# Kernel optimization log

Measured on AMD Instinct MI355X. Metric: run time of the kernel, lower is better.

The kernel has to match this reference:

```python
import jax, jax.numpy as jnp
import numpy as np

K_TOP = 2
N_HEADS = 4

def _ln(x, g, b, eps=1e-5):
    mu = x.mean(-1, keepdims=True)
    var = ((x - mu) ** 2).mean(-1, keepdims=True)
    return (x - mu) * jax.lax.rsqrt(var + eps) * g + b

def setup_inputs() -> dict:
    key = jax.random.key(0)
    ks = jax.random.split(key, 12)
    B, Na, dz, da = 1024, 32, 96, 32
    D = dz + da
    E, F, Hh, nr = 8, 1024, 512, 4
    s = 0.02
    rn = lambda k, sh: jax.random.normal(k, sh, jnp.float32) * s
    return dict(
        z=jax.random.normal(ks[0], (B, Na, dz), jnp.float32),
        a=jax.random.normal(ks[1], (B, Na, da), jnp.float32),
        w_gate=rn(ks[2], (Na * D, E)),
        w_in=rn(ks[3], (E, 3 * D, D)), b_in=jnp.zeros((E, 3 * D), jnp.float32),
        w_out=rn(ks[4], (E, D, D)), b_out=jnp.zeros((E, D), jnp.float32),
        ln1_g=jnp.ones((E, D), jnp.float32), ln1_b=jnp.zeros((E, D), jnp.float32),
        w1=rn(ks[5], (E, F, D)), b1=jnp.zeros((E, F), jnp.float32),
        w2=rn(ks[6], (E, D, F)), b2=jnp.zeros((E, D), jnp.float32),
        ln2_g=jnp.ones((E, D), jnp.float32), ln2_b=jnp.zeros((E, D), jnp.float32),
        head_w1=rn(ks[7], (Hh, Na * D)), head_b1=jnp.zeros((Hh,), jnp.float32),
        head_w2=rn(ks[8], (nr, Hh)), head_b2=jnp.zeros((nr,), jnp.float32),
    )

def reference(z, a, w_gate, w_in, b_in, w_out, b_out, ln1_g, ln1_b, w1, b1, w2, b2, ln2_g, ln2_b, head_w1, head_b1, head_w2, head_b2):
    B, Na, _ = z.shape
    x = jnp.concatenate([z, a], axis=-1)          # [B, Na, D]
    D = x.shape[-1]
    E = w_gate.shape[1]
    hd = D // N_HEADS
    x_flat = x.reshape(B, -1)                     # [B, Na*D]

    # --- NoisyTopKRouter (eval: clean logits only) ---
    logits = x_flat @ w_gate                      # [B, E]
    top_vals, top_idx = jax.lax.top_k(logits, min(K_TOP + 1, E))
    tk_gates = jax.nn.softmax(top_vals[:, :K_TOP], axis=1)
    gates = jnp.zeros_like(logits).at[jnp.arange(B)[:, None], top_idx[:, :K_TOP]].set(tk_gates)
    load = (gates > 0).sum(0).astype(jnp.float32)
    importance = gates.sum(0)
    cv2 = lambda v: jnp.var(v, ddof=1) / (jnp.mean(v) ** 2 + 1e-10)
    loss_bal = cv2(importance) + cv2(load) + jax.scipy.special.logsumexp(logits, axis=-1).mean()

    # --- expert (self-attn + FFN, pre/post-LN residual) ---
    def expert(p):
        wi, bi, wo, bo, g1, be1, W1, B1, W2, B2, g2, be2 = p
        qkv = x @ wi.T + bi                       # [B, Na, 3D]
        q, k_, v = jnp.split(qkv, 3, axis=-1)
        q = q.reshape(B, Na, N_HEADS, hd)
        k_ = k_.reshape(B, Na, N_HEADS, hd)
        v = v.reshape(B, Na, N_HEADS, hd)
        sc = jnp.einsum('bqhd,bkhd->bhqk', q, k_) / jnp.sqrt(jnp.float32(hd))
        att = jax.nn.softmax(sc, axis=-1)
        o = jnp.einsum('bhqk,bkhd->bqhd', att, v).reshape(B, Na, D)
        o = o @ wo.T + bo
        h = _ln(x + o, g1, be1)
        f = jax.nn.relu(h @ W1.T + B1) @ W2.T + B2
        return _ln(h + f, g2, be2)

    def body(y, p):
        *ep, gate_e = p                           # gate_e: [B]
        y = y + gate_e[:, None, None] * expert(tuple(ep))
        return y, None

    xs = (w_in, b_in, w_out, b_out, ln1_g, ln1_b, w1, b1, w2, b2, ln2_g, ln2_b, gates.T)
    y, _ = jax.lax.scan(body, jnp.zeros_like(x), xs)

    y_flat = y.reshape(B, -1)
    r = jax.nn.relu(y_flat @ head_w1.T + head_b1) @ head_w2.T + head_b2  # [B, n_r]
    return r, gates, loss_bal
```

## Files before the change

### kernel.cpp

```cpp
#include <hip/hip_runtime.h>
#include <math.h>


typedef short bf16x8 __attribute__((ext_vector_type(8)));
typedef float f32x4 __attribute__((ext_vector_type(4)));
typedef unsigned short u16;

#define MFMA(a, b, c) __builtin_amdgcn_mfma_f32_16x16x32_bf16((a), (b), (c), 0, 0, 0)

__device__ __forceinline__ u16 f2bf(float f) {
    unsigned int u = __float_as_uint(f);
    unsigned int r = u + 0x7FFFu + ((u >> 16) & 1u);
    return (u16)(r >> 16);
}
__device__ __forceinline__ float bf2f(u16 s) {
    return __uint_as_float(((unsigned int)s) << 16);
}

__global__ __launch_bounds__(256) void convert_kernel(
    const float* __restrict__ wi, const float* __restrict__ wo,
    const float* __restrict__ w1, const float* __restrict__ w2,
    const float* __restrict__ hw1,
    u16* __restrict__ wiB, u16* __restrict__ woB, u16* __restrict__ w1B,
    u16* __restrict__ w2B, u16* __restrict__ hw1B)
{
    int i4 = blockIdx.x * 256 + threadIdx.x;
    int e = i4 * 4;
    const float* s; u16* d; int off;
    if (e < 393216)       { s = wi;  d = wiB;  off = e; }
    else if (e < 524288)  { s = wo;  d = woB;  off = e - 393216; }
    else if (e < 1572864) { s = w1;  d = w1B;  off = e - 524288; }
    else if (e < 2621440) { s = w2;  d = w2B;  off = e - 1572864; }
    else                  { s = hw1; d = hw1B; off = e - 2621440; }
    float4 v = *(const float4*)(s + off);
    ushort4 o;
    o.x = f2bf(v.x); o.y = f2bf(v.y); o.z = f2bf(v.z); o.w = f2bf(v.w);
    *(ushort4*)(d + off) = o;
}

__global__ __launch_bounds__(256) void router_kernel(
    const float* __restrict__ z, const float* __restrict__ a,
    const float* __restrict__ wg,
    float* __restrict__ gates_out, float* __restrict__ lse_ws,
    int* __restrict__ topi, float* __restrict__ topg)
{
    __shared__ float red[256][9];
    const int b = blockIdx.x, t = threadIdx.x;
    float acc[8];
#pragma unroll
    for (int e = 0; e < 8; ++e) acc[e] = 0.f;
#pragma unroll
    for (int i = 0; i < 16; ++i) {
        int f = i * 256 + t;
        int n = f >> 7, d = f & 127;
        float xv = (d < 96) ? z[(b * 32 + n) * 96 + d]
                            : a[(b * 32 + n) * 32 + d - 96];
        const float* wr = wg + f * 8;
#pragma unroll
        for (int e = 0; e < 8; ++e) acc[e] += xv * wr[e];
    }
#pragma unroll
    for (int e = 0; e < 8; ++e) red[t][e] = acc[e];
    __syncthreads();
    for (int s = 128; s; s >>= 1) {
        if (t < s) {
#pragma unroll
            for (int e = 0; e < 8; ++e) red[t][e] += red[t + s][e];
        }
        __syncthreads();
    }
    if (t == 0) {
        float L[8];
#pragma unroll
        for (int e = 0; e < 8; ++e) L[e] = red[0][e];
        int i0 = 0;
#pragma unroll
        for (int e = 1; e < 8; ++e) if (L[e] > L[i0]) i0 = e;
        int i1 = -1; float v1 = -3.0e38f;
#pragma unroll
        for (int e = 0; e < 8; ++e) if (e != i0 && L[e] > v1) { v1 = L[e]; i1 = e; }
        float e1 = expf(v1 - L[i0]);
        float inv = 1.f / (1.f + e1);
        float g0 = inv, g1 = e1 * inv;
#pragma unroll
        for (int e = 0; e < 8; ++e)
            gates_out[b * 8 + e] = (e == i0) ? g0 : ((e == i1) ? g1 : 0.f);
        float m = L[i0];
        float se = 0.f;
#pragma unroll
        for (int e = 0; e < 8; ++e) se += expf(L[e] - m);
        lse_ws[b] = m + logf(se);
        topi[b * 2 + 0] = i0; topi[b * 2 + 1] = i1;
        topg[b * 2 + 0] = g0; topg[b * 2 + 1] = g1;
    }
}

__global__ __launch_bounds__(1024) void build_loss_kernel(
    const int* __restrict__ topi, const float* __restrict__ topg,
    const float* __restrict__ lse,
    int* __restrict__ cnts, int* __restrict__ ent, float* __restrict__ out_loss)
{
    __shared__ int sc_[8];
    __shared__ float red[9][1024];
    const int t = threadIdx.x;
    if (t < 8) sc_[t] = 0;
    __syncthreads();
    int e0 = topi[t * 2], e1 = topi[t * 2 + 1];
    float g0 = topg[t * 2], g1 = topg[t * 2 + 1];
    int p0 = atomicAdd(&sc_[e0], 1);
    ent[e0 * 2048 + p0] = t * 2;
    int p1 = atomicAdd(&sc_[e1], 1);
    ent[e1 * 2048 + p1] = t * 2 + 1;
#pragma unroll
    for (int e = 0; e < 8; ++e)
        red[e][t] = ((e == e0) ? g0 : 0.f) + ((e == e1) ? g1 : 0.f);
    red[8][t] = lse[t];
    __syncthreads();
    for (int s = 512; s; s >>= 1) {
        if (t < s) {
#pragma unroll
            for (int q = 0; q < 9; ++q) red[q][t] += red[q][t + s];
        }
        __syncthreads();
    }
    if (t == 0) {
        float cvv[2];
        for (int p = 0; p < 2; ++p) {
            float v[8], sum = 0.f;
            for (int e = 0; e < 8; ++e) {
                v[e] = p ? (float)sc_[e] : red[e][0];
                sum += v[e];
            }
            float mean = sum * (1.f / 8.f);
            float var = 0.f;
            for (int e = 0; e < 8; ++e) { float d = v[e] - mean; var += d * d; }
            var *= (1.f / 7.f);
            cvv[p] = var / (mean * mean + 1e-10f);
        }
        out_loss[0] = cvv[0] + cvv[1] + red[8][0] * (1.f / 1024.f);
    }
    __syncthreads();
    if (t < 8) cnts[t] = sc_[t];
}

#define SM_X 0
#define SM_Q 16384
#define SM_K 32768
#define SM_V 49152
#define SM_TOT 65536
#define PS_OFF 0
#define PQ_OFF 1024
#define MU_OFF 2048
#define RS_OFF 2304
#define ATTN_GRID 8192

__device__ __forceinline__ int tsw(int row, int col) {
    return row * 256 + ((col * 2) ^ ((row & 7) << 4));
}
__device__ __forceinline__ int vsw(int row, int col) {
    return row * 128 + ((col * 2) ^ ((row & 7) << 4));
}

__global__ __launch_bounds__(512, 2) void attn_kernel(
    const float* __restrict__ z, const float* __restrict__ a,
    const u16* __restrict__ wiBF, const float* __restrict__ b_in,
    const u16* __restrict__ woBF, const float* __restrict__ b_out,
    const float* __restrict__ ln1g, const float* __restrict__ ln1b,
    const int* __restrict__ cnts, const int* __restrict__ ent,
    u16* __restrict__ h1g)
{
    const int e = blockIdx.x & 7, j = blockIdx.x >> 3;
    const int cnt = cnts[e];
    if (j * 2 >= cnt) return;
    const int base = j * 2;

    __shared__ __align__(16) char sm[SM_TOT];
    const int t = threadIdx.x;
    const int w = t >> 6, l = t & 63, l16 = l & 15, lk = l >> 4;
    const int ke = lk * 8;
    const int wr = w >> 2, wc = w & 3;
    const f32x4 zv = {0.f, 0.f, 0.f, 0.f};

    int bs[2];
#pragma unroll
    for (int i = 0; i < 2; ++i) {
        int gi = base + i;
        int idx = (gi < cnt) ? gi : (cnt - 1);
        bs[i] = ent[e * 2048 + idx];
    }

#pragma unroll
    for (int i = 0; i < 2; ++i) {
        int cid = i * 512 + t;
        int row = cid >> 4;
        int cb = (cid & 15) * 8;
        int b_ = bs[row >> 5] >> 1;
        int n = row & 31;
        float4 p0, p1;
        if (cb < 96) {
            const float* zp = z + ((size_t)b_ * 32 + n) * 96 + cb;
            p0 = *(const float4*)zp; p1 = *(const float4*)(zp + 4);
        } else {
            const float* ap = a + ((size_t)b_ * 32 + n) * 32 + (cb - 96);
            p0 = *(const float4*)ap; p1 = *(const float4*)(ap + 4);
        }
        bf16x8 pk;
        pk[0] = (short)f2bf(p0.x); pk[1] = (short)f2bf(p0.y);
        pk[2] = (short)f2bf(p0.z); pk[3] = (short)f2bf(p0.w);
        pk[4] = (short)f2bf(p1.x); pk[5] = (short)f2bf(p1.y);
        pk[6] = (short)f2bf(p1.z); pk[7] = (short)f2bf(p1.w);
        *(bf16x8*)(sm + SM_X + tsw(row, cb)) = pk;
    }
    __syncthreads();

    {
        f32x4 acc[2][6];
#pragma unroll
        for (int mt = 0; mt < 2; ++mt)
#pragma unroll
            for (int q = 0; q < 6; ++q) acc[mt][q] = zv;
#pragma unroll
        for (int ks = 0; ks < 4; ++ks) {
            bf16x8 af[2];
#pragma unroll
            for (int mt = 0; mt < 2; ++mt) {
                int R = wr * 32 + mt * 16 + l16;
                af[mt] = *(const bf16x8*)(sm + SM_X + tsw(R, ks * 32 + ke));
            }
#pragma unroll
            for (int q = 0; q < 6; ++q) {
                int jj = wc * 96 + q * 16 + l16;
                bf16x8 bb = *(const bf16x8*)(wiBF + e * 49152 + jj * 128 + ks * 32 + ke);
#pragma unroll
                for (int mt = 0; mt < 2; ++mt) acc[mt][q] = MFMA(af[mt], bb, acc[mt][q]);
            }
        }
#pragma unroll
        for (int q = 0; q < 6; ++q) {
            int C = wc * 96 + q * 16 + l16;
            float bj = b_in[e * 384 + C];
#pragma unroll
            for (int mt = 0; mt < 2; ++mt)
#pragma unroll
                for (int i = 0; i < 4; ++i) {
                    int R = wr * 32 + mt * 16 + lk * 4 + i;
                    u16 val = f2bf(acc[mt][q][i] + bj);
                    if (C < 128) {
                        *(u16*)(sm + SM_Q + tsw(R, C)) = val;
                    } else if (C < 256) {
                        *(u16*)(sm + SM_K + tsw(R, C - 128)) = val;
                    } else {
                        *(u16*)(sm + SM_V + vsw(C - 256, R)) = val;
                    }
                }
        }
    }
    __syncthreads();

    {
        const int tok = w >> 2, hb = (w & 3) * 32;
        const float scale = 0.17677669529663687f;
        bf16x8 qa[2], kf[2];
#pragma unroll
        for (int mt = 0; mt < 2; ++mt) {
            int R = tok * 32 + mt * 16 + l16;
            qa[mt] = *(const bf16x8*)(sm + SM_Q + tsw(R, hb + ke));
            kf[mt] = *(const bf16x8*)(sm + SM_K + tsw(R, hb + ke));
        }
        f32x4 sc[2][2];
        sc[0][0] = MFMA(qa[0], kf[0], zv); sc[0][1] = MFMA(qa[0], kf[1], zv);
        sc[1][0] = MFMA(qa[1], kf[0], zv); sc[1][1] = MFMA(qa[1], kf[1], zv);
#pragma unroll
        for (int mt = 0; mt < 2; ++mt)
#pragma unroll
            for (int i = 0; i < 4; ++i) {
                float v0 = sc[mt][0][i] * scale, v1 = sc[mt][1][i] * scale;
                float m = fmaxf(v0, v1);
                m = fmaxf(m, __shfl_xor(m, 1)); m = fmaxf(m, __shfl_xor(m, 2));
                m = fmaxf(m, __shfl_xor(m, 4)); m = fmaxf(m, __shfl_xor(m, 8));
                float e0 = __expf(v0 - m), e1 = __expf(v1 - m);
                float ssum = e0 + e1;
                ssum += __shfl_xor(ssum, 1); ssum += __shfl_xor(ssum, 2);
                ssum += __shfl_xor(ssum, 4); ssum += __shfl_xor(ssum, 8);
                float inv = 1.f / ssum;
                int row = mt * 16 + lk * 4 + i;
                char* pb = sm + SM_X + w * 2048 + row * 64;
                int sw = (row & 3) << 4;
                *(u16*)(pb + ((l16 * 2) ^ sw)) = f2bf(e0 * inv);
                *(u16*)(pb + (((16 + l16) * 2) ^ sw)) = f2bf(e1 * inv);
            }
        bf16x8 pa[2];
#pragma unroll
        for (int mt = 0; mt < 2; ++mt) {
            int row = mt * 16 + l16;
            pa[mt] = *(const bf16x8*)(sm + SM_X + w * 2048 + row * 64 +
                                      ((ke * 2) ^ ((row & 3) << 4)));
        }
        f32x4 o[2][2];
#pragma unroll
        for (int nt = 0; nt < 2; ++nt) {
            int rv = hb + nt * 16 + l16;
            bf16x8 vb = *(const bf16x8*)(sm + SM_V + vsw(rv, tok * 32 + ke));
            o[0][nt] = MFMA(pa[0], vb, zv);
            o[1][nt] = MFMA(pa[1], vb, zv);
        }
#pragma unroll
        for (int mt = 0; mt < 2; ++mt)
#pragma unroll
            for (int nt = 0; nt < 2; ++nt)
#pragma unroll
                for (int i = 0; i < 4; ++i) {
                    int R = tok * 32 + mt * 16 + lk * 4 + i;
                    int C = hb + nt * 16 + l16;
                    *(u16*)(sm + SM_Q + tsw(R, C)) = f2bf(o[mt][nt][i]);
                }
    }
    __syncthreads();

    {
        f32x4 pr[2][2];
        pr[0][0] = zv; pr[0][1] = zv; pr[1][0] = zv; pr[1][1] = zv;
#pragma unroll
        for (int ks = 0; ks < 4; ++ks) {
            bf16x8 af[2];
#pragma unroll
            for (int mt = 0; mt < 2; ++mt) {
                int R = wr * 32 + mt * 16 + l16;
                af[mt] = *(const bf16x8*)(sm + SM_Q + tsw(R, ks * 32 + ke));
            }
#pragma unroll
            for (int nt = 0; nt < 2; ++nt) {
                int jj = wc * 32 + nt * 16 + l16;
                bf16x8 bb = *(const bf16x8*)(woBF + e * 16384 + jj * 128 + ks * 32 + ke);
                pr[0][nt] = MFMA(af[0], bb, pr[0][nt]);
                pr[1][nt] = MFMA(af[1], bb, pr[1][nt]);
            }
        }
        int C0 = wc * 32 + l16, C1 = C0 + 16;
        float bo0 = b_out[e * 128 + C0];
        float bo1 = b_out[e * 128 + C1];
        int b_ = bs[wr] >> 1;
#pragma unroll
        for (int mt = 0; mt < 2; ++mt)
#pragma unroll
            for (int i = 0; i < 4; ++i) {
                int R = wr * 32 + mt * 16 + lk * 4 + i;
                int n = R & 31;
                float x0 = (C0 < 96) ? z[((size_t)b_ * 32 + n) * 96 + C0]
                                     : a[((size_t)b_ * 32 + n) * 32 + C0 - 96];
                float x1 = (C1 < 96) ? z[((size_t)b_ * 32 + n) * 96 + C1]
                                     : a[((size_t)b_ * 32 + n) * 32 + C1 - 96];
                float u0 = pr[mt][0][i] + bo0 + x0;
                float u1v = pr[mt][1][i] + bo1 + x1;
                *(u16*)(sm + SM_K + tsw(R, C0)) = f2bf(u0);
                *(u16*)(sm + SM_K + tsw(R, C1)) = f2bf(u1v);
                float s = u0 + u1v;
                float q = u0 * u0 + u1v * u1v;
                s += __shfl_xor(s, 1); q += __shfl_xor(q, 1);
                s += __shfl_xor(s, 2); q += __shfl_xor(q, 2);
                s += __shfl_xor(s, 4); q += __shfl_xor(q, 4);
                s += __shfl_xor(s, 8); q += __shfl_xor(q, 8);
                if (l16 == 0) {
                    *(float*)(sm + SM_X + PS_OFF + (R * 4 + wc) * 4) = s;
                    *(float*)(sm + SM_X + PQ_OFF + (R * 4 + wc) * 4) = q;
                }
            }
    }
    __syncthreads();
    if (t < 64) {
        float s = 0.f, q = 0.f;
#pragma unroll
        for (int c = 0; c < 4; ++c) {
            s += *(const float*)(sm + SM_X + PS_OFF + (t * 4 + c) * 4);
            q += *(const float*)(sm + SM_X + PQ_OFF + (t * 4 + c) * 4);
        }
        float mu = s * (1.f / 128.f);
        float var = q * (1.f / 128.f) - mu * mu;
        *(float*)(sm + SM_X + MU_OFF + t * 4) = mu;
        *(float*)(sm + SM_X + RS_OFF + t * 4) = rsqrtf(var + 1e-5f);
    }
    __syncthreads();
    {
        int r_ = t >> 3, c0 = (t & 7) * 16;
        float mu_ = *(const float*)(sm + SM_X + MU_OFF + r_ * 4);
        float rs_ = *(const float*)(sm + SM_X + RS_OFF + r_ * 4);
#pragma unroll
        for (int j4 = 0; j4 < 2; ++j4) {
            int cb = c0 + j4 * 8;
            bf16x8* p = (bf16x8*)(sm + SM_K + tsw(r_, cb));
            bf16x8 vch = *p;
#pragma unroll
            for (int jj = 0; jj < 8; ++jj) {
                int c = cb + jj;
                float f = (bf2f((u16)vch[jj]) - mu_) * rs_ * ln1g[e * 128 + c] + ln1b[e * 128 + c];
                vch[jj] = (short)f2bf(f);
            }
            *p = vch;
        }
    }
    __syncthreads();
#pragma unroll
    for (int i = 0; i < 2; ++i) {
        int cid = i * 512 + t;
        int r_ = cid >> 4, cb = (cid & 15) * 8;
        int code = bs[r_ >> 5];
        u16* dst = h1g + (size_t)code * 4096 + (r_ & 31) * 128 + cb;
        *(bf16x8*)dst = *(const bf16x8*)(sm + SM_K + tsw(r_, cb));
    }
}

#define FH 0
#define FF 32768
#define FPS 65536
#define FPQ 67584
#define FMU 69632
#define FRS 70144
#define F_TOT 70656
#define FFN_GRID 4096

__global__ __launch_bounds__(512, 2) void ffn_kernel(
    const u16* __restrict__ h1g,
    const u16* __restrict__ w1BF, const float* __restrict__ b1,
    const u16* __restrict__ w2BF, const float* __restrict__ b2,
    const float* __restrict__ ln2g, const float* __restrict__ ln2b,
    const float* __restrict__ topg, const int* __restrict__ cnts,
    const int* __restrict__ ent,
    u16* __restrict__ ybf)
{
    const int e = blockIdx.x & 7, jt = blockIdx.x >> 3;
    const int cnt = cnts[e];
    if (jt * 4 >= cnt) return;
    const int base = jt * 4;

    __shared__ __align__(16) char sm[F_TOT];
    const int t = threadIdx.x;
    const int w = t >> 6, l = t & 63, l16 = l & 15, lk = l >> 4;
    const int ke = lk * 8;
    const int wr = w >> 2, wc = w & 3;
    const f32x4 zv = {0.f, 0.f, 0.f, 0.f};

    int code4[4]; float gg4[4];
#pragma unroll
    for (int i = 0; i < 4; ++i) {
        int gi = base + i;
        int idx = (gi < cnt) ? gi : (cnt - 1);
        code4[i] = ent[e * 2048 + idx];
        gg4[i] = topg[code4[i]];
    }

#pragma unroll
    for (int it = 0; it < 4; ++it) {
        int cid = it * 512 + t;
        int row = cid >> 4, cb = (cid & 15) * 8;
        int code = code4[row >> 5];
        *(bf16x8*)(sm + FH + tsw(row, cb)) =
            *(const bf16x8*)(h1g + (size_t)code * 4096 + (row & 31) * 128 + cb);
    }
    __syncthreads();

    f32x4 facc[4][2];
#pragma unroll
    for (int mt = 0; mt < 4; ++mt) { facc[mt][0] = zv; facc[mt][1] = zv; }

    for (int c = 0; c < 8; ++c) {
        f32x4 a1[4][2];
#pragma unroll
        for (int mt = 0; mt < 4; ++mt) { a1[mt][0] = zv; a1[mt][1] = zv; }
#pragma unroll
        for (int ks = 0; ks < 4; ++ks) {
            bf16x8 af[4];
#pragma unroll
            for (int mt = 0; mt < 4; ++mt) {
                int R = wr * 64 + mt * 16 + l16;
                af[mt] = *(const bf16x8*)(sm + FH + tsw(R, ks * 32 + ke));
            }
#pragma unroll
            for (int nt = 0; nt < 2; ++nt) {
                int jj = c * 128 + wc * 32 + nt * 16 + l16;
                bf16x8 bb = *(const bf16x8*)(w1BF + e * 131072 + jj * 128 + ks * 32 + ke);
#pragma unroll
                for (int mt = 0; mt < 4; ++mt) a1[mt][nt] = MFMA(af[mt], bb, a1[mt][nt]);
            }
        }
        __syncthreads();
#pragma unroll
        for (int nt = 0; nt < 2; ++nt) {
            int C = wc * 32 + nt * 16 + l16;
            float bv = b1[e * 1024 + c * 128 + C];
#pragma unroll
            for (int mt = 0; mt < 4; ++mt)
#pragma unroll
                for (int i = 0; i < 4; ++i) {
                    int R = wr * 64 + mt * 16 + lk * 4 + i;
                    *(u16*)(sm + FF + tsw(R, C)) = f2bf(fmaxf(a1[mt][nt][i] + bv, 0.f));
                }
        }
        __syncthreads();
#pragma unroll
        for (int ks = 0; ks < 4; ++ks) {
            bf16x8 af[4];
#pragma unroll
            for (int mt = 0; mt < 4; ++mt) {
                int R = wr * 64 + mt * 16 + l16;
                af[mt] = *(const bf16x8*)(sm + FF + tsw(R, ks * 32 + ke));
            }
#pragma unroll
            for (int nt = 0; nt < 2; ++nt) {
                int jj = wc * 32 + nt * 16 + l16;
                bf16x8 bb = *(const bf16x8*)(w2BF + e * 131072 + jj * 1024 +
                                             c * 128 + ks * 32 + ke);
#pragma unroll
                for (int mt = 0; mt < 4; ++mt) facc[mt][nt] = MFMA(af[mt], bb, facc[mt][nt]);
            }
        }
    }
    __syncthreads();

    {
        int C0 = wc * 32 + l16, C1 = C0 + 16;
        float b20 = b2[e * 128 + C0];
        float b21 = b2[e * 128 + C1];
#pragma unroll
        for (int mt = 0; mt < 4; ++mt)
#pragma unroll
            for (int i = 0; i < 4; ++i) {
                int R = wr * 64 + mt * 16 + lk * 4 + i;
                float h0 = bf2f(*(const u16*)(sm + FH + tsw(R, C0)));
                float h1v = bf2f(*(const u16*)(sm + FH + tsw(R, C1)));
                float u0 = facc[mt][0][i] + b20 + h0;
                float u1v = facc[mt][1][i] + b21 + h1v;
                *(u16*)(sm + FF + tsw(R, C0)) = f2bf(u0);
                *(u16*)(sm + FF + tsw(R, C1)) = f2bf(u1v);
                float s = u0 + u1v;
                float q = u0 * u0 + u1v * u1v;
                s += __shfl_xor(s, 1); q += __shfl_xor(q, 1);
                s += __shfl_xor(s, 2); q += __shfl_xor(q, 2);
                s += __shfl_xor(s, 4); q += __shfl_xor(q, 4);
                s += __shfl_xor(s, 8); q += __shfl_xor(q, 8);
                if (l16 == 0) {
                    *(float*)(sm + FPS + (R * 4 + wc) * 4) = s;
                    *(float*)(sm + FPQ + (R * 4 + wc) * 4) = q;
                }
            }
    }
    __syncthreads();
    if (t < 128) {
        float s = 0.f, q = 0.f;
#pragma unroll
        for (int c = 0; c < 4; ++c) {
            s += *(const float*)(sm + FPS + (t * 4 + c) * 4);
            q += *(const float*)(sm + FPQ + (t * 4 + c) * 4);
        }
        float mu = s * (1.f / 128.f);
        float var = q * (1.f / 128.f) - mu * mu;
        *(float*)(sm + FMU + t * 4) = mu;
        *(float*)(sm + FRS + t * 4) = rsqrtf(var + 1e-5f);
    }
    __syncthreads();
#pragma unroll
    for (int it = 0; it < 4; ++it) {
        int cid = it * 512 + t;
        int row = cid >> 4, cb = (cid & 15) * 8;
        float mu = *(const float*)(sm + FMU + row * 4);
        float rs = *(const float*)(sm + FRS + row * 4);
        int ei = row >> 5;
        float gm = gg4[ei];
        int code = code4[ei];
        int tok = code >> 1, slot = code & 1;
        bf16x8 v = *(const bf16x8*)(sm + FF + tsw(row, cb));
        bf16x8 o;
#pragma unroll
        for (int jj = 0; jj < 8; ++jj) {
            int cc = cb + jj;
            float f = (bf2f((u16)v[jj]) - mu) * rs * ln2g[e * 128 + cc] + ln2b[e * 128 + cc];
            o[jj] = (short)f2bf(gm * f);
        }
        *(bf16x8*)(ybf + (size_t)(slot * 1024 + tok) * 4096 + (row & 31) * 128 + cb) = o;
    }
}

__global__ __launch_bounds__(256) void combine_kernel(
    u16* __restrict__ y0, const u16* __restrict__ y1)
{
    int i = (blockIdx.x * 256 + threadIdx.x) * 8;
    bf16x8 a = *(const bf16x8*)(y0 + i);
    bf16x8 b = *(const bf16x8*)(y1 + i);
    bf16x8 o;
#pragma unroll
    for (int j = 0; j < 8; ++j)
        o[j] = (short)f2bf(bf2f((u16)a[j]) + bf2f((u16)b[j]));
    *(bf16x8*)(y0 + i) = o;
}

__global__ __launch_bounds__(256) void head1_mfma(
    const u16* __restrict__ y_bf, const u16* __restrict__ hw1BF,
    const float* __restrict__ hb1, float* __restrict__ h_act)
{
    const int t = threadIdx.x, w = t >> 6, l = t & 63, l16 = l & 15, lk = l >> 4;
    const int ke = lk * 8;
    const int mb = blockIdx.x * 32, cb = blockIdx.y * 64 + w * 16;
    const f32x4 zv = {0.f, 0.f, 0.f, 0.f};
    f32x4 acc[2]; acc[0] = zv; acc[1] = zv;
    const u16* arow0 = y_bf + (size_t)(mb + l16) * 4096;
    const u16* arow1 = y_bf + (size_t)(mb + 16 + l16) * 4096;
    const u16* brow  = hw1BF + (size_t)(cb + l16) * 4096;
    for (int k0 = 0; k0 < 4096; k0 += 32) {
        bf16x8 a0 = *(const bf16x8*)(arow0 + k0 + ke);
        bf16x8 a1 = *(const bf16x8*)(arow1 + k0 + ke);
        bf16x8 bb = *(const bf16x8*)(brow + k0 + ke);
        acc[0] = MFMA(a0, bb, acc[0]);
        acc[1] = MFMA(a1, bb, acc[1]);
    }
    int col = cb + l16;
    float bv = hb1[col];
#pragma unroll
    for (int mt = 0; mt < 2; ++mt)
#pragma unroll
        for (int i = 0; i < 4; ++i) {
            int row = mb + mt * 16 + lk * 4 + i;
            h_act[(size_t)row * 512 + col] = fmaxf(acc[mt][i] + bv, 0.f);
        }
}

__global__ __launch_bounds__(64) void head2_kernel(
    const float* __restrict__ h_act, const float* __restrict__ w2,
    const float* __restrict__ b2, float* __restrict__ r)
{
    const int b = blockIdx.x, t = threadIdx.x;
    float a0 = 0.f, a1 = 0.f, a2 = 0.f, a3 = 0.f;
    for (int h = t; h < 512; h += 64) {
        float hv = h_act[b * 512 + h];
        a0 += hv * w2[h];
        a1 += hv * w2[512 + h];
        a2 += hv * w2[1024 + h];
        a3 += hv * w2[1536 + h];
    }
#pragma unroll
    for (int off = 32; off; off >>= 1) {
        a0 += __shfl_down(a0, off);
        a1 += __shfl_down(a1, off);
        a2 += __shfl_down(a2, off);
        a3 += __shfl_down(a3, off);
    }
    if (t == 0) {
        r[b * 4 + 0] = a0 + b2[0];
        r[b * 4 + 1] = a1 + b2[1];
        r[b * 4 + 2] = a2 + b2[2];
        r[b * 4 + 3] = a3 + b2[3];
    }
}

extern "C" void kernel_launch(void* const* d_in, const int* in_sizes, int n_in,
                              void* d_out, int out_size, void* d_ws, size_t ws_size,
                              hipStream_t stream) {
    const float* z    = (const float*)d_in[0];
    const float* a    = (const float*)d_in[1];
    const float* wg   = (const float*)d_in[2];
    const float* w_in = (const float*)d_in[3];
    const float* b_in = (const float*)d_in[4];
    const float* w_o  = (const float*)d_in[5];
    const float* b_o  = (const float*)d_in[6];
    const float* l1g  = (const float*)d_in[7];
    const float* l1b  = (const float*)d_in[8];
    const float* w1   = (const float*)d_in[9];
    const float* b1   = (const float*)d_in[10];
    const float* w2   = (const float*)d_in[11];
    const float* b2   = (const float*)d_in[12];
    const float* l2g  = (const float*)d_in[13];
    const float* l2b  = (const float*)d_in[14];
    const float* hw1  = (const float*)d_in[15];
    const float* hb1  = (const float*)d_in[16];
    const float* hw2  = (const float*)d_in[17];
    const float* hb2  = (const float*)d_in[18];

    float* out = (float*)d_out;
    float* r_out     = out;
    float* gates_out = out + 4096;
    float* loss_out  = out + 12288;

    char* W = (char*)d_ws;
    u16*   wiBF  = (u16*)(W + 0);
    u16*   woBF  = (u16*)(W + 786432);
    u16*   w1BF  = (u16*)(W + 1048576);
    u16*   w2BF  = (u16*)(W + 3145728);
    u16*   hw1BF = (u16*)(W + 5242880);
    u16*   ybf   = (u16*)(W + 9437184);
    u16*   h1g   = (u16*)(W + 26214400);
    float* h_act = (float*)(W + 42991616);
    float* lse   = (float*)(W + 45088768);
    float* topg  = (float*)(W + 45092864);
    int*   topi  = (int*)  (W + 45101056);
    int*   cnts  = (int*)  (W + 45109248);
    int*   ent   = (int*)  (W + 45109376);

    convert_kernel<<<4608, 256, 0, stream>>>(w_in, w_o, w1, w2, hw1,
                                             wiBF, woBF, w1BF, w2BF, hw1BF);
    router_kernel<<<1024, 256, 0, stream>>>(z, a, wg, gates_out, lse, topi, topg);
    build_loss_kernel<<<1, 1024, 0, stream>>>(topi, topg, lse, cnts, ent, loss_out);
    attn_kernel<<<ATTN_GRID, 512, 0, stream>>>(z, a, wiBF, b_in, woBF, b_o,
        l1g, l1b, cnts, ent, h1g);
    ffn_kernel<<<FFN_GRID, 512, 0, stream>>>(h1g, w1BF, b1, w2BF, b2,
        l2g, l2b, topg, cnts, ent, ybf);
    combine_kernel<<<2048, 256, 0, stream>>>(ybf, ybf + 4194304);
    head1_mfma<<<dim3(32, 8), 256, 0, stream>>>(ybf, hw1BF, hb1, h_act);
    head2_kernel<<<1024, 64, 0, stream>>>(h_act, hw2, hb2, r_out);
}
```

Before: 320.9 us.

## Restructure FFN kernel to keep full 1024-wide hidden activations in LDS

The FFN kernel now handles 2 entries (64 rows) per block instead of 4 (128 rows). It computes the whole 64x1024 ReLU hidden layer into shared memory in one pass, with each wave owning 128 hidden columns, and then runs the second GEMM over K=1024 without the per-chunk barriers. This removes the two __syncthreads per hidden chunk and the interleaving of the two GEMMs. The cost is about 146KB of LDS per block, so occupancy drops to one block per CU despite launch_bounds(512,2). Each block also reuses its streamed weights across half as many rows, which doubles total weight traffic.

After: 322.9 us. Within noise of the previous version (+0.6%).

```diff
diff --git a/kernel.cpp b/kernel.cpp
--- a/kernel.cpp
+++ b/kernel.cpp
@@ -159,6 +159,9 @@
 }
 __device__ __forceinline__ int vsw(int row, int col) {
     return row * 128 + ((col * 2) ^ ((row & 7) << 4));
+}
+__device__ __forceinline__ int fsw(int row, int col) {
+    return row * 2048 + ((col * 2) ^ ((row & 7) << 4));
 }
 
 __global__ __launch_bounds__(512, 2) void attn_kernel(
@@ -410,13 +413,13 @@
 }
 
 #define FH 0
-#define FF 32768
-#define FPS 65536
-#define FPQ 67584
-#define FMU 69632
-#define FRS 70144
-#define F_TOT 70656
-#define FFN_GRID 4096
+#define FFB 16384
+#define FPS 147456
+#define FPQ 148480
+#define FMU 149504
+#define FRS 149760
+#define F_TOT 150016
+#define FFN_GRID 8192
 
 __global__ __launch_bounds__(512, 2) void ffn_kernel(
     const u16* __restrict__ h1g,
@@ -429,8 +432,8 @@
 {
     const int e = blockIdx.x & 7, jt = blockIdx.x >> 3;
     const int cnt = cnts[e];
-    if (jt * 4 >= cnt) return;
-    const int base = jt * 4;
+    if (jt * 2 >= cnt) return;
+    const int base = jt * 2;
 
     __shared__ __align__(16) char sm[F_TOT];
     const int t = threadIdx.x;
@@ -439,79 +442,75 @@
     const int wr = w >> 2, wc = w & 3;
     const f32x4 zv = {0.f, 0.f, 0.f, 0.f};
 
-    int code4[4]; float gg4[4];
-#pragma unroll
-    for (int i = 0; i < 4; ++i) {
+    int code2[2]; float gg2[2];
+#pragma unroll
+    for (int i = 0; i < 2; ++i) {
         int gi = base + i;
         int idx = (gi < cnt) ? gi : (cnt - 1);
-        code4[i] = ent[e * 2048 + idx];
-        gg4[i] = topg[code4[i]];
-    }
-
-#pragma unroll
-    for (int it = 0; it < 4; ++it) {
+        code2[i] = ent[e * 2048 + idx];
+        gg2[i] = topg[code2[i]];
+    }
+
+#pragma unroll
+    for (int it = 0; it < 2; ++it) {
         int cid = it * 512 + t;
         int row = cid >> 4, cb = (cid & 15) * 8;
-        int code = code4[row >> 5];
+        int code = code2[row >> 5];
         *(bf16x8*)(sm + FH + tsw(row, cb)) =
             *(const bf16x8*)(h1g + (size_t)code * 4096 + (row & 31) * 128 + cb);
     }
     __syncthreads();
 
-    f32x4 facc[4][2];
-#pragma unroll
-    for (int mt = 0; mt < 4; ++mt) { facc[mt][0] = zv; facc[mt][1] = zv; }
-
-    for (int c = 0; c < 8; ++c) {
-        f32x4 a1[4][2];
-#pragma unroll
-        for (int mt = 0; mt < 4; ++mt) { a1[mt][0] = zv; a1[mt][1] = zv; }
+    for (int h = 0; h < 4; ++h) {
+        f32x4 acc[4][2];
+#pragma unroll
+        for (int mf = 0; mf < 4; ++mf) { acc[mf][0] = zv; acc[mf][1] = zv; }
 #pragma unroll
         for (int ks = 0; ks < 4; ++ks) {
             bf16x8 af[4];
 #pragma unroll
-            for (int mt = 0; mt < 4; ++mt) {
-                int R = wr * 64 + mt * 16 + l16;
-                af[mt] = *(const bf16x8*)(sm + FH + tsw(R, ks * 32 + ke));
-            }
-#pragma unroll
-            for (int nt = 0; nt < 2; ++nt) {
-                int jj = c * 128 + wc * 32 + nt * 16 + l16;
+            for (int mf = 0; mf < 4; ++mf) {
+                int R = mf * 16 + l16;
+                af[mf] = *(const bf16x8*)(sm + FH + tsw(R, ks * 32 + ke));
+            }
+#pragma unroll
+            for (int nf = 0; nf < 2; ++nf) {
+                int jj = w * 128 + h * 32 + nf * 16 + l16;
                 bf16x8 bb = *(const bf16x8*)(w1BF + e * 131072 + jj * 128 + ks * 32 + ke);
 #pragma unroll
-                for (int mt = 0; mt < 4; ++mt) a1[mt][nt] = MFMA(af[mt], bb, a1[mt][nt]);
-            }
-        }
-        __syncthreads();
-#pragma unroll
-        for (int nt = 0; nt < 2; ++nt) {
-            int C = wc * 32 + nt * 16 + l16;
-            float bv = b1[e * 1024 + c * 128 + C];
-#pragma unroll
-            for (int mt = 0; mt < 4; ++mt)
+                for (int mf = 0; mf < 4; ++mf) acc[mf][nf] = MFMA(af[mf], bb, acc[mf][nf]);
+            }
+        }
+#pragma unroll
+        for (int nf = 0; nf < 2; ++nf) {
+            int C = w * 128 + h * 32 + nf * 16 + l16;
+            float bv = b1[e * 1024 + C];
+#pragma unroll
+            for (int mf = 0; mf < 4; ++mf)
 #pragma unroll
                 for (int i = 0; i < 4; ++i) {
-                    int R = wr * 64 + mt * 16 + lk * 4 + i;
-                    *(u16*)(sm + FF + tsw(R, C)) = f2bf(fmaxf(a1[mt][nt][i] + bv, 0.f));
+                    int R = mf * 16 + lk * 4 + i;
+                    *(u16*)(sm + FFB + fsw(R, C)) = f2bf(fmaxf(acc[mf][nf][i] + bv, 0.f));
                 }
         }
-        __syncthreads();
-#pragma unroll
-        for (int ks = 0; ks < 4; ++ks) {
-            bf16x8 af[4];
-#pragma unroll
-            for (int mt = 0; mt < 4; ++mt) {
-                int R = wr * 64 + mt * 16 + l16;
-                af[mt] = *(const bf16x8*)(sm + FF + tsw(R, ks * 32 + ke));
-            }
-#pragma unroll
-            for (int nt = 0; nt < 2; ++nt) {
-                int jj = wc * 32 + nt * 16 + l16;
-                bf16x8 bb = *(const bf16x8*)(w2BF + e * 131072 + jj * 1024 +
-                                             c * 128 + ks * 32 + ke);
-#pragma unroll
-                for (int mt = 0; mt < 4; ++mt) facc[mt][nt] = MFMA(af[mt], bb, facc[mt][nt]);
-            }
+    }
+    __syncthreads();
+
+    f32x4 cacc[2][2];
+    cacc[0][0] = zv; cacc[0][1] = zv; cacc[1][0] = zv; cacc[1][1] = zv;
+    for (int ks = 0; ks < 32; ++ks) {
+        bf16x8 af[2];
+#pragma unroll
+        for (int mt = 0; mt < 2; ++mt) {
+            int R = wr * 32 + mt * 16 + l16;
+            af[mt] = *(const bf16x8*)(sm + FFB + fsw(R, ks * 32 + ke));
+        }
+#pragma unroll
+        for (int nf = 0; nf < 2; ++nf) {
+            int jj = wc * 32 + nf * 16 + l16;
+            bf16x8 bb = *(const bf16x8*)(w2BF + e * 131072 + jj * 1024 + ks * 32 + ke);
+            cacc[0][nf] = MFMA(af[0], bb, cacc[0][nf]);
+            cacc[1][nf] = MFMA(af[1], bb, cacc[1][nf]);
         }
     }
     __syncthreads();
@@ -521,16 +520,16 @@
         float b20 = b2[e * 128 + C0];
         float b21 = b2[e * 128 + C1];
 #pragma unroll
-        for (int mt = 0; mt < 4; ++mt)
+        for (int mt = 0; mt < 2; ++mt)
 #pragma unroll
             for (int i = 0; i < 4; ++i) {
-                int R = wr * 64 + mt * 16 + lk * 4 + i;
+                int R = wr * 32 + mt * 16 + lk * 4 + i;
                 float h0 = bf2f(*(const u16*)(sm + FH + tsw(R, C0)));
                 float h1v = bf2f(*(const u16*)(sm + FH + tsw(R, C1)));
-                float u0 = facc[mt][0][i] + b20 + h0;
-                float u1v = facc[mt][1][i] + b21 + h1v;
-                *(u16*)(sm + FF + tsw(R, C0)) = f2bf(u0);
-                *(u16*)(sm + FF + tsw(R, C1)) = f2bf(u1v);
+                float u0 = cacc[mt][0][i] + b20 + h0;
+                float u1v = cacc[mt][1][i] + b21 + h1v;
+                *(u16*)(sm + FFB + tsw(R, C0)) = f2bf(u0);
+                *(u16*)(sm + FFB + tsw(R, C1)) = f2bf(u1v);
                 float s = u0 + u1v;
                 float q = u0 * u0 + u1v * u1v;
                 s += __shfl_xor(s, 1); q += __shfl_xor(q, 1);
@@ -544,7 +543,7 @@
             }
     }
     __syncthreads();
-    if (t < 128) {
+    if (t < 64) {
         float s = 0.f, q = 0.f;
 #pragma unroll
         for (int c = 0; c < 4; ++c) {
@@ -558,16 +557,16 @@
     }
     __syncthreads();
 #pragma unroll
-    for (int it = 0; it < 4; ++it) {
+    for (int it = 0; it < 2; ++it) {
         int cid = it * 512 + t;
         int row = cid >> 4, cb = (cid & 15) * 8;
         float mu = *(const float*)(sm + FMU + row * 4);
         float rs = *(const float*)(sm + FRS + row * 4);
         int ei = row >> 5;
-        float gm = gg4[ei];
-        int code = code4[ei];
+        float gm = gg2[ei];
+        int code = code2[ei];
         int tok = code >> 1, slot = code & 1;
-        bf16x8 v = *(const bf16x8*)(sm + FF + tsw(row, cb));
+        bf16x8 v = *(const bf16x8*)(sm + FFB + tsw(row, cb));
         bf16x8 o;
 #pragma unroll
         for (int jj = 0; jj < 8; ++jj) {
```
